# Optimization experiments

Hardware: AMD Instinct MI355X
Metric: run time of the kernel (lower is better)

Reference implementation:

```python
import jax, jax.numpy as jnp
import numpy as np

S, L, D = 128, 512, 256   # MSA rows, residues, msa_dim
H, C = 8, 32              # num_heads, head_dim


def setup_inputs() -> dict:
    key = jax.random.key(0)
    ks = jax.random.split(key, 8)
    inp = {
        "msa_input": jax.random.normal(ks[0], (S, L, D), dtype=jnp.float32),
        "ln_scale": jnp.ones((D,), jnp.float32),
        "ln_bias": jnp.zeros((D,), jnp.float32),
        "wq": jax.random.normal(ks[1], (D, H * C), jnp.float32) / np.sqrt(D),
        "wk": jax.random.normal(ks[2], (D, H * C), jnp.float32) / np.sqrt(D),
        "wv": jax.random.normal(ks[3], (D, H * C), jnp.float32) / np.sqrt(D),
        "wg": jax.random.normal(ks[4], (D, H * C), jnp.float32) / np.sqrt(D),
        "bg": jnp.zeros((H * C,), jnp.float32),
        "wo": jax.random.normal(ks[5], (H * C, D), jnp.float32) / np.sqrt(H * C),
        "bo": jnp.zeros((D,), jnp.float32),
    }
    return inp


def reference(msa_input, ln_scale, ln_bias, wq, wk, wv, wg, bg, wo, bo):
    # LayerNorm over last dim (eps matches torch default 1e-5)
    mu = jnp.mean(msa_input, axis=-1, keepdims=True)
    var = jnp.mean(jnp.square(msa_input - mu), axis=-1, keepdims=True)
    x = (msa_input - mu) * jax.lax.rsqrt(var + 1e-5) * ln_scale + ln_bias

    q = (x @ wq).reshape(S, L, H, C)
    k = (x @ wk).reshape(S, L, H, C)
    v = (x @ wv).reshape(S, L, H, C)
    g = jax.nn.sigmoid(x @ wg + bg).reshape(S, L, H, C)

    scale = 1.0 / np.sqrt(C)
    # attention over MSA-row axis, per residue l and head h
    scores = jnp.einsum("slhc,tlhc->stlh", q, k) * scale   # [S,S,L,H]
    probs = jax.nn.softmax(scores, axis=1)                  # softmax over t
    o = jnp.einsum("stlh,tlhc->slhc", probs, v) * g         # [S,L,H,C]
    return o.reshape(S, L, H * C) @ wo + bo
```

## Files before the change

kernel.cpp:

```cpp
#include <hip/hip_runtime.h>
#include <hip/hip_bf16.h>

typedef __bf16 bf16;
typedef __bf16 bf16x8 __attribute__((ext_vector_type(8)));
typedef float f32x4 __attribute__((ext_vector_type(4)));

#define S_DIM 128
#define L_DIM 512
#define D_DIM 256
#define NQ    1024

__device__ __forceinline__ void gl16(void* lds, const void* g) {
  __builtin_amdgcn_global_load_lds((const __attribute__((address_space(1))) void*)g,
                                   (__attribute__((address_space(3))) void*)lds,
                                   16, 0, 0);
}

__global__ void pack_weights(const float* __restrict__ wq, const float* __restrict__ wk,
                             const float* __restrict__ wv, const float* __restrict__ wg,
                             const float* __restrict__ wo,
                             bf16* __restrict__ wcat_t, bf16* __restrict__ wo_t) {
  int idx = blockIdx.x * 256 + threadIdx.x;
  const int total1 = NQ * D_DIM;
  if (idx < total1) {
    int j = idx >> 8;
    int d = idx & 255;
    const float* w = (j < 256) ? wq : (j < 512) ? wk : (j < 768) ? wv : wg;
    wcat_t[idx] = (bf16)w[d * 256 + (j & 255)];
  } else {
    int i2 = idx - total1;
    if (i2 < D_DIM * D_DIM) {
      int dcol = i2 >> 8, k = i2 & 255;
      wo_t[i2] = (bf16)wo[k * 256 + dcol];
    }
  }
}

__global__ __launch_bounds__(512, 4) void ln_qkvg(const float* __restrict__ msa,
                                                  const float* __restrict__ lns,
                                                  const float* __restrict__ lnb,
                                                  const bf16* __restrict__ wcat,
                                                  const float* __restrict__ bg,
                                                  bf16* __restrict__ pan) {
  __shared__ __align__(16) char smem[65536];
  bf16* Albs = (bf16*)smem;
  char* Bb   = smem;
  const int tid  = threadIdx.x;
  const int wid  = tid >> 6;
  const int lane = tid & 63;
  const int lrow = lane & 15;
  const int lkg  = lane >> 4;
  const int lk   = lkg * 8;
  const int rb   = lkg * 4;
  const int res  = blockIdx.x;

  {
    float4 scv = ((const float4*)lns)[lane];
    float4 bsv = ((const float4*)lnb)[lane];
    const float* mbase = msa + ((size_t)(wid * 16) * 512 + res) * 256 + lane * 4;
    #pragma unroll
    for (int b4 = 0; b4 < 4; ++b4) {
      float4 rv[4];
      #pragma unroll
      for (int i = 0; i < 4; ++i)
        rv[i] = *(const float4*)(mbase + (size_t)(b4 * 4 + i) * 512 * 256);
      #pragma unroll
      for (int i = 0; i < 4; ++i) {
        int s = wid * 16 + b4 * 4 + i;
        float4 v = rv[i];
        float sum = v.x + v.y + v.z + v.w;
        #pragma unroll
        for (int m = 32; m; m >>= 1) sum += __shfl_xor(sum, m);
        float mu = sum * (1.0f / 256.0f);
        float dx = v.x - mu, dy = v.y - mu, dz = v.z - mu, dw = v.w - mu;
        float s2 = dx * dx + dy * dy + dz * dz + dw * dw;
        #pragma unroll
        for (int m = 32; m; m >>= 1) s2 += __shfl_xor(s2, m);
        float rs = rsqrtf(s2 * (1.0f / 256.0f) + 1e-5f);
        union { uint2 u; bf16 b[4]; } o;
        o.b[0] = (bf16)(dx * rs * scv.x + bsv.x);
        o.b[1] = (bf16)(dy * rs * scv.y + bsv.y);
        o.b[2] = (bf16)(dz * rs * scv.z + bsv.z);
        o.b[3] = (bf16)(dw * rs * scv.w + bsv.w);
        *(uint2*)((char*)Albs + (((s * 512) + lane * 8) ^ ((s & 7) << 4))) = o.u;
      }
    }
  }
  __syncthreads();

  const int mq = wid & 3;
  const int nh = wid >> 2;
  bf16x8 afc[2][8];
  #pragma unroll
  for (int mt = 0; mt < 2; ++mt)
    #pragma unroll
    for (int kk = 0; kk < 8; ++kk) {
      int row = mq * 32 + mt * 16 + lrow;
      afc[mt][kk] = *(const bf16x8*)((char*)Albs +
                      (((row * 512) + (kk * 32 + lk) * 2) ^ ((row & 7) << 4)));
    }
  __syncthreads();

  #pragma unroll
  for (int p = 0; p < 4; ++p) {
    int ch = p * 512 + tid;
    int n = ch >> 5;
    int inner = (ch & 31) * 16;
    gl16(Bb + p * 8192 + wid * 1024,
         (const char*)wcat + (size_t)n * 512 + (inner ^ ((n & 7) << 4)));
  }
  __syncthreads();

  const int tb = (mq * 32 + rb) * 64 + nh * 32 + lrow;

  #pragma unroll 1
  for (int cc = 0; cc < 16; ++cc) {
    char* Bcur = Bb + (cc & 1) * 32768;
    if (cc < 15) {
      char* Bnxt = Bb + ((cc + 1) & 1) * 32768;
      const size_t ncol0 = (size_t)(cc + 1) * 64;
      #pragma unroll
      for (int p = 0; p < 4; ++p) {
        int ch = p * 512 + tid;
        int n = ch >> 5;
        int inner = (ch & 31) * 16;
        gl16(Bnxt + p * 8192 + wid * 1024,
             (const char*)wcat + (ncol0 + n) * 512 + (inner ^ ((n & 7) << 4)));
      }
    }
    f32x4 acc[2][2] = {};
    #pragma unroll
    for (int kk = 0; kk < 8; ++kk) {
      bf16x8 bv[2];
      #pragma unroll
      for (int nt = 0; nt < 2; ++nt) {
        int nl = nh * 32 + nt * 16 + lrow;
        bv[nt] = *(const bf16x8*)(Bcur +
                    (((nl * 512) + (kk * 32 + lk) * 2) ^ ((nl & 7) << 4)));
      }
      #pragma unroll
      for (int mt = 0; mt < 2; ++mt)
        #pragma unroll
        for (int nt = 0; nt < 2; ++nt)
          acc[mt][nt] = __builtin_amdgcn_mfma_f32_16x16x32_bf16(afc[mt][kk], bv[nt], acc[mt][nt], 0, 0, 0);
    }
    {
      const bool isg = (cc >= 12);
      const int type = cc >> 2, hp = cc & 3;
      bf16* pstore = pan + ((size_t)((type * 512 + res) * 4) + hp) * 8192 + tb;
      float bgv[2];
      if (isg) {
        bgv[0] = bg[(cc - 12) * 64 + nh * 32 + lrow];
        bgv[1] = bg[(cc - 12) * 64 + nh * 32 + 16 + lrow];
      }
      #pragma unroll
      for (int mt = 0; mt < 2; ++mt)
        #pragma unroll
        for (int nt = 0; nt < 2; ++nt)
          #pragma unroll
          for (int r = 0; r < 4; ++r) {
            float v = acc[mt][nt][r];
            if (isg) { v += bgv[nt]; v = 1.0f / (1.0f + __expf(-v)); }
            pstore[mt * 1024 + r * 64 + nt * 16] = (bf16)v;
          }
    }
    if (cc < 15) {
      asm volatile("s_waitcnt vmcnt(16) lgkmcnt(0)" ::: "memory");
      __builtin_amdgcn_s_barrier();
    }
  }
}

__global__ __launch_bounds__(256, 4) void attn_kernel(const bf16* __restrict__ pan,
                                                      bf16* __restrict__ obuf) {
  __shared__ __align__(16) char smem[40960];
  const int tid  = threadIdx.x;
  const int wid  = tid >> 6;
  const int lane = tid & 63;
  const int lrow = lane & 15;
  const int lkg  = lane >> 4;
  const int lk   = lkg * 8;
  const int rb   = lkg * 4;
  const int bid  = blockIdx.x;
  const int rest = bid >> 3;
  const int hg   = rest & 1;
  const int res  = (bid & 7) | ((rest >> 1) << 3);
  const int h    = hg * 4 + wid;
  const int hp   = h >> 1;
  const int hl   = (h & 1) * 32;

  char* vw  = smem + wid * 8192;
  char* pwb = smem + 32768 + wid * 2048;

  const bf16* Pq = pan + ((size_t)((0 * 512 + res) * 4) + hp) * 8192 + hl;
  const bf16* Pk = pan + ((size_t)((1 * 512 + res) * 4) + hp) * 8192 + hl;
  const bf16* Pv = pan + ((size_t)((2 * 512 + res) * 4) + hp) * 8192 + hl;
  const bf16* Pg = pan + ((size_t)((3 * 512 + res) * 4) + hp) * 8192 + hl;

  {
    int t0 = lane >> 2, cs = (lane & 3) * 8;
    #pragma unroll
    for (int p = 0; p < 8; ++p) {
      int t = p * 16 + t0;
      union { uint4 u; bf16 e[8]; } v;
      v.u = *(const uint4*)(Pv + t * 64 + cs);
      #pragma unroll
      for (int j = 0; j < 8; ++j) {
        int c = cs + j;
        *(bf16*)(vw + ((c * 256 + t * 2) ^ ((c & 7) << 4))) = v.e[j];
      }
    }
  }

  bf16x8 kf[8];
  #pragma unroll
  for (int tt = 0; tt < 8; ++tt)
    kf[tt] = *(const bf16x8*)(Pk + (tt * 16 + lrow) * 64 + lk);

  const float scale = 0.17677669529663687f;
  const f32x4 z = {0.f, 0.f, 0.f, 0.f};

  for (int st = 0; st < 8; ++st) {
    bf16x8 qf = *(const bf16x8*)(Pq + (st * 16 + lrow) * 64 + lk);
    f32x4 sc[8];
    #pragma unroll
    for (int tt = 0; tt < 8; ++tt)
      sc[tt] = __builtin_amdgcn_mfma_f32_16x16x32_bf16(qf, kf[tt], z, 0, 0, 0);

    #pragma unroll
    for (int r = 0; r < 4; ++r) {
      float m = sc[0][r];
      #pragma unroll
      for (int tc = 1; tc < 8; ++tc) m = fmaxf(m, sc[tc][r]);
      #pragma unroll
      for (int msk = 8; msk; msk >>= 1) m = fmaxf(m, __shfl_xor(m, msk));
      float pv[8], ssum = 0.f;
      #pragma unroll
      for (int tc = 0; tc < 8; ++tc) {
        float p = __expf((sc[tc][r] - m) * scale);
        pv[tc] = p; ssum += p;
      }
      #pragma unroll
      for (int msk = 8; msk; msk >>= 1) ssum += __shfl_xor(ssum, msk);
      float inv = 1.0f / ssum;
      #pragma unroll
      for (int tc = 0; tc < 8; ++tc) sc[tc][r] = pv[tc] * inv;
    }

    f32x4 oc[2] = {z, z};
    #pragma unroll
    for (int hf = 0; hf < 2; ++hf) {
      #pragma unroll
      for (int tc = 0; tc < 4; ++tc)
        #pragma unroll
        for (int r = 0; r < 4; ++r) {
          int row = rb + r, col = tc * 16 + lrow;
          *(bf16*)(pwb + ((row * 128 + col * 2) ^ ((row & 7) << 4))) = (bf16)sc[hf * 4 + tc][r];
        }
      #pragma unroll
      for (int kc = 0; kc < 2; ++kc) {
        bf16x8 pa = *(const bf16x8*)(pwb + ((lrow * 128 + (kc * 32 + lk) * 2) ^ ((lrow & 7) << 4)));
        #pragma unroll
        for (int ct = 0; ct < 2; ++ct) {
          int c = ct * 16 + lrow;
          bf16x8 bv = *(const bf16x8*)(vw + ((c * 256 + (hf * 64 + kc * 32 + lk) * 2) ^ ((c & 7) << 4)));
          oc[ct] = __builtin_amdgcn_mfma_f32_16x16x32_bf16(pa, bv, oc[ct], 0, 0, 0);
        }
      }
    }

    #pragma unroll
    for (int ct = 0; ct < 2; ++ct)
      #pragma unroll
      for (int r = 0; r < 4; ++r) {
        int row = rb + r, c = ct * 16 + lrow;
        *(bf16*)(pwb + ((row * 128 + c * 2) ^ ((row & 7) << 4))) = (bf16)oc[ct][r];
      }
    {
      int row = lane >> 2, cb = lane & 3;
      union { uint4 u; bf16 e[8]; } o8, g8, r8;
      o8.u = *(const uint4*)(pwb + ((row * 128 + cb * 16) ^ ((row & 7) << 4)));
      g8.u = *(const uint4*)(Pg + (st * 16 + row) * 64 + cb * 8);
      #pragma unroll
      for (int u = 0; u < 8; ++u) r8.e[u] = (bf16)((float)o8.e[u] * (float)g8.e[u]);
      *(uint4*)(obuf + ((size_t)res * 128 + st * 16 + row) * 256 + h * 32 + cb * 8) = r8.u;
    }
  }
}

__global__ __launch_bounds__(256, 4) void gemm_proj(const bf16* __restrict__ A,
                                                    const bf16* __restrict__ Bt,
                                                    float* __restrict__ Cout,
                                                    const float* __restrict__ bias) {
  __shared__ __align__(16) bf16 smem[16384];
  bf16* As = smem;
  bf16* Bs = smem + 8192;
  const int tid  = threadIdx.x;
  const int wid  = tid >> 6;
  const int lane = tid & 63;
  const int bid   = blockIdx.x;
  const int n_idx = (bid >> 3) & 1;
  const int m_idx = (bid & 7) | ((bid >> 4) << 3);
  const int m0 = m_idx * 128;
  const int n0 = n_idx * 128;
  const int lrow = lane & 15;
  const int lk   = (lane >> 4) * 8;
  const int wr = wid >> 1, wc = wid & 1;

  const int ln8 = lane >> 3;
  const int c8  = ((lane & 7) ^ ln8) * 8;

  const bf16* Arow = A  + (size_t)m0 * 256 + c8;
  const bf16* Brow = Bt + (size_t)n0 * 256 + c8;

  f32x4 acc[4][4] = {};

  #pragma unroll
  for (int ks = 0; ks < 4; ++ks) {
    const int k0 = ks * 64;
    #pragma unroll
    for (int t = 0; t < 4; ++t) {
      int chunk = wid * 4 + t;
      int r = chunk * 8 + ln8;
      gl16(&As[chunk * 512], Arow + (size_t)r * 256 + k0);
      gl16(&Bs[chunk * 512], Brow + (size_t)r * 256 + k0);
    }
    __syncthreads();
    #pragma unroll
    for (int kk = 0; kk < 64; kk += 32) {
      bf16x8 av[4], bv[4];
      #pragma unroll
      for (int i = 0; i < 4; ++i)
        av[i] = *(const bf16x8*)((const char*)As + ((((wr * 64 + i * 16 + lrow) * 128) + (kk + lk) * 2) ^ (((wr * 64 + i * 16 + lrow) & 7) << 4)));
      #pragma unroll
      for (int j = 0; j < 4; ++j)
        bv[j] = *(const bf16x8*)((const char*)Bs + ((((wc * 64 + j * 16 + lrow) * 128) + (kk + lk) * 2) ^ (((wc * 64 + j * 16 + lrow) & 7) << 4)));
      #pragma unroll
      for (int i = 0; i < 4; ++i)
        #pragma unroll
        for (int j = 0; j < 4; ++j)
          acc[i][j] = __builtin_amdgcn_mfma_f32_16x16x32_bf16(av[i], bv[j], acc[i][j], 0, 0, 0);
    }
    __syncthreads();
  }

  const int rb = (lane >> 4) * 4;
  const int xorv = rb << 2;
  float* smf = (float*)smem;
  float bov[4];
  #pragma unroll
  for (int j = 0; j < 4; ++j) bov[j] = bias[n0 + wc * 64 + j * 16 + lrow];
  #pragma unroll
  for (int half = 0; half < 2; ++half) {
    if (half) __syncthreads();
    #pragma unroll
    for (int i2 = 0; i2 < 2; ++i2) {
      int i = half * 2 + i2;
      #pragma unroll
      for (int j = 0; j < 4; ++j) {
        int col = wc * 64 + j * 16 + lrow;
        #pragma unroll
        for (int r = 0; r < 4; ++r) {
          int crow = wr * 32 + i2 * 16 + rb + r;
          smf[crow * 128 + (col ^ xorv)] = acc[i][j][r] + bov[j];
        }
      }
    }
    __syncthreads();
    #pragma unroll
    for (int p = 0; p < 8; ++p) {
      int ch = p * 256 + tid;
      int crow = ch >> 5, slot = (ch & 31) * 4;
      int rx = (crow & 12) << 2;
      int s_loc = (crow >> 5) * 64 + half * 32 + (crow & 31);
      *(uint4*)(Cout + ((size_t)s_loc * 512 + m_idx) * 256 + n0 + slot) =
          *(const uint4*)(smf + crow * 128 + (slot ^ rx));
    }
  }
}

extern "C" void kernel_launch(void* const* d_in, const int* in_sizes, int n_in,
                              void* d_out, int out_size, void* d_ws, size_t ws_size,
                              hipStream_t stream) {
  const float* msa      = (const float*)d_in[0];
  const float* ln_scale = (const float*)d_in[1];
  const float* ln_bias  = (const float*)d_in[2];
  const float* wq       = (const float*)d_in[3];
  const float* wk       = (const float*)d_in[4];
  const float* wv       = (const float*)d_in[5];
  const float* wg       = (const float*)d_in[6];
  const float* bg       = (const float*)d_in[7];
  const float* wo       = (const float*)d_in[8];
  const float* bo       = (const float*)d_in[9];
  float* out = (float*)d_out;

  char* ws = (char*)d_ws;
  bf16* wcat_t = (bf16*)ws;
  bf16* wo_t   = (bf16*)(ws + 524288);
  bf16* pan    = (bf16*)(ws + 655360);
  bf16* obuf   = (bf16*)(ws + 655360 + 134217728ULL);

  pack_weights<<<dim3(1280), dim3(256), 0, stream>>>(wq, wk, wv, wg, wo, wcat_t, wo_t);
  ln_qkvg<<<dim3(512), dim3(512), 0, stream>>>(msa, ln_scale, ln_bias, wcat_t, bg, pan);
  attn_kernel<<<dim3(1024), dim3(256), 0, stream>>>(pan, obuf);
  gemm_proj<<<dim3(1024), dim3(256), 0, stream>>>(obuf, wo_t, out, bo);
}
```

Baseline: 141.1 us.

## Split fused LayerNorm+QKVG kernel into separate LN pass and tiled GEMM

Replaces the fused per-residue LayerNorm+QKVG projection kernel with two kernels. A standalone LN kernel writes bf16 normalized rows, transposed to residue-major, into the output buffer as scratch. A conventional 256x64-tiled GEMM with global-to-LDS loads then computes Q/K/V/G over 4096 blocks. This trades the fused kernel's register-resident A fragments and weight streaming for better parallelism, at the cost of an extra bf16 round trip through global memory and one more kernel launch.

```diff
diff --git a/kernel.cpp b/kernel.cpp
--- a/kernel.cpp
+++ b/kernel.cpp
@@ -36,15 +36,45 @@
   }
 }
 
-__global__ __launch_bounds__(512, 4) void ln_qkvg(const float* __restrict__ msa,
-                                                  const float* __restrict__ lns,
-                                                  const float* __restrict__ lnb,
-                                                  const bf16* __restrict__ wcat,
-                                                  const float* __restrict__ bg,
-                                                  bf16* __restrict__ pan) {
-  __shared__ __align__(16) char smem[65536];
-  bf16* Albs = (bf16*)smem;
-  char* Bb   = smem;
+__global__ __launch_bounds__(256) void ln_kernel(const float* __restrict__ x,
+                                                 const float* __restrict__ sc,
+                                                 const float* __restrict__ bs,
+                                                 bf16* __restrict__ y) {
+  int wid  = threadIdx.x >> 6;
+  int lane = threadIdx.x & 63;
+  int row  = blockIdx.x * 4 + wid;
+  float4 v = ((const float4*)(x + (size_t)row * D_DIM))[lane];
+  float s = v.x + v.y + v.z + v.w;
+  #pragma unroll
+  for (int m = 32; m; m >>= 1) s += __shfl_xor(s, m);
+  float mu = s * (1.0f / 256.0f);
+  float dx = v.x - mu, dy = v.y - mu, dz = v.z - mu, dw = v.w - mu;
+  float s2 = dx * dx + dy * dy + dz * dz + dw * dw;
+  #pragma unroll
+  for (int m = 32; m; m >>= 1) s2 += __shfl_xor(s2, m);
+  float rs = rsqrtf(s2 * (1.0f / 256.0f) + 1e-5f);
+  float4 scv = ((const float4*)sc)[lane];
+  float4 bsv = ((const float4*)bs)[lane];
+  union { uint2 u; bf16 b[4]; } o;
+  o.b[0] = (bf16)(dx * rs * scv.x + bsv.x);
+  o.b[1] = (bf16)(dy * rs * scv.y + bsv.y);
+  o.b[2] = (bf16)(dz * rs * scv.z + bsv.z);
+  o.b[3] = (bf16)(dw * rs * scv.w + bsv.w);
+  int sr = row >> 9, l = row & 511;
+  ((uint2*)y)[(size_t)(l * 128 + sr) * 64 + lane] = o.u;
+}
+
+__device__ __forceinline__ bf16x8 lds_swz(const char* base, int row, int k) {
+  return *(const bf16x8*)(base + (((row << 7) + (k << 1)) ^ ((row & 7) << 4)));
+}
+
+__global__ __launch_bounds__(512, 4) void gemm_qkvg(const bf16* __restrict__ A,
+                                                    const bf16* __restrict__ Bt,
+                                                    bf16* __restrict__ pan,
+                                                    const float* __restrict__ bias) {
+  __shared__ __align__(16) char smem[40960];
+  char* As = smem;
+  char* Bs = smem + 32768;
   const int tid  = threadIdx.x;
   const int wid  = tid >> 6;
   const int lane = tid & 63;
@@ -52,122 +82,71 @@
   const int lkg  = lane >> 4;
   const int lk   = lkg * 8;
   const int rb   = lkg * 4;
-  const int res  = blockIdx.x;
+  const int bid  = blockIdx.x;
+  const int n_idx = (bid >> 3) & 15;
+  const int m_idx = (bid & 7) | ((bid >> 7) << 3);
+  const int m0 = m_idx * 256;
+  const int n0 = n_idx * 64;
+  const int rg = wid >> 1;
+  const int cg = wid & 1;
+
+  const int srow8 = tid >> 3;
+  const int slot  = tid & 7;
+
+  f32x4 acc[4][2] = {};
+
+  #pragma unroll
+  for (int ks = 0; ks < 4; ++ks) {
+    const int k0 = ks * 64;
+    #pragma unroll
+    for (int p = 0; p < 4; ++p) {
+      int r = p * 64 + srow8;
+      gl16(As + p * 8192 + wid * 1024,
+           A + (size_t)(m0 + r) * 256 + k0 + ((slot ^ (r & 7)) * 8));
+    }
+    gl16(Bs + wid * 1024,
+         Bt + (size_t)(n0 + srow8) * 256 + k0 + ((slot ^ (srow8 & 7)) * 8));
+    __syncthreads();
+    #pragma unroll
+    for (int kk = 0; kk < 64; kk += 32) {
+      bf16x8 av[4], bv[2];
+      #pragma unroll
+      for (int i = 0; i < 4; ++i)
+        av[i] = lds_swz(As, rg * 64 + i * 16 + lrow, kk + lk);
+      #pragma unroll
+      for (int nt = 0; nt < 2; ++nt)
+        bv[nt] = lds_swz(Bs, cg * 32 + nt * 16 + lrow, kk + lk);
+      #pragma unroll
+      for (int i = 0; i < 4; ++i)
+        #pragma unroll
+        for (int nt = 0; nt < 2; ++nt)
+          acc[i][nt] = __builtin_amdgcn_mfma_f32_16x16x32_bf16(av[i], bv[nt], acc[i][nt], 0, 0, 0);
+    }
+    if (ks < 3) __syncthreads();
+  }
 
   {
-    float4 scv = ((const float4*)lns)[lane];
-    float4 bsv = ((const float4*)lnb)[lane];
-    const float* mbase = msa + ((size_t)(wid * 16) * 512 + res) * 256 + lane * 4;
-    #pragma unroll
-    for (int b4 = 0; b4 < 4; ++b4) {
-      float4 rv[4];
-      #pragma unroll
-      for (int i = 0; i < 4; ++i)
-        rv[i] = *(const float4*)(mbase + (size_t)(b4 * 4 + i) * 512 * 256);
-      #pragma unroll
-      for (int i = 0; i < 4; ++i) {
-        int s = wid * 16 + b4 * 4 + i;
-        float4 v = rv[i];
-        float sum = v.x + v.y + v.z + v.w;
-        #pragma unroll
-        for (int m = 32; m; m >>= 1) sum += __shfl_xor(sum, m);
-        float mu = sum * (1.0f / 256.0f);
-        float dx = v.x - mu, dy = v.y - mu, dz = v.z - mu, dw = v.w - mu;
-        float s2 = dx * dx + dy * dy + dz * dz + dw * dw;
-        #pragma unroll
-        for (int m = 32; m; m >>= 1) s2 += __shfl_xor(s2, m);
-        float rs = rsqrtf(s2 * (1.0f / 256.0f) + 1e-5f);
-        union { uint2 u; bf16 b[4]; } o;
-        o.b[0] = (bf16)(dx * rs * scv.x + bsv.x);
-        o.b[1] = (bf16)(dy * rs * scv.y + bsv.y);
-        o.b[2] = (bf16)(dz * rs * scv.z + bsv.z);
-        o.b[3] = (bf16)(dw * rs * scv.w + bsv.w);
-        *(uint2*)((char*)Albs + (((s * 512) + lane * 8) ^ ((s & 7) << 4))) = o.u;
-      }
-    }
-  }
-  __syncthreads();
-
-  const int mq = wid & 3;
-  const int nh = wid >> 2;
-  bf16x8 afc[2][8];
-  #pragma unroll
-  for (int mt = 0; mt < 2; ++mt)
-    #pragma unroll
-    for (int kk = 0; kk < 8; ++kk) {
-      int row = mq * 32 + mt * 16 + lrow;
-      afc[mt][kk] = *(const bf16x8*)((char*)Albs +
-                      (((row * 512) + (kk * 32 + lk) * 2) ^ ((row & 7) << 4)));
-    }
-  __syncthreads();
-
-  #pragma unroll
-  for (int p = 0; p < 4; ++p) {
-    int ch = p * 512 + tid;
-    int n = ch >> 5;
-    int inner = (ch & 31) * 16;
-    gl16(Bb + p * 8192 + wid * 1024,
-         (const char*)wcat + (size_t)n * 512 + (inner ^ ((n & 7) << 4)));
-  }
-  __syncthreads();
-
-  const int tb = (mq * 32 + rb) * 64 + nh * 32 + lrow;
-
-  #pragma unroll 1
-  for (int cc = 0; cc < 16; ++cc) {
-    char* Bcur = Bb + (cc & 1) * 32768;
-    if (cc < 15) {
-      char* Bnxt = Bb + ((cc + 1) & 1) * 32768;
-      const size_t ncol0 = (size_t)(cc + 1) * 64;
-      #pragma unroll
-      for (int p = 0; p < 4; ++p) {
-        int ch = p * 512 + tid;
-        int n = ch >> 5;
-        int inner = (ch & 31) * 16;
-        gl16(Bnxt + p * 8192 + wid * 1024,
-             (const char*)wcat + (ncol0 + n) * 512 + (inner ^ ((n & 7) << 4)));
-      }
-    }
-    f32x4 acc[2][2] = {};
-    #pragma unroll
-    for (int kk = 0; kk < 8; ++kk) {
-      bf16x8 bv[2];
-      #pragma unroll
-      for (int nt = 0; nt < 2; ++nt) {
-        int nl = nh * 32 + nt * 16 + lrow;
-        bv[nt] = *(const bf16x8*)(Bcur +
-                    (((nl * 512) + (kk * 32 + lk) * 2) ^ ((nl & 7) << 4)));
-      }
-      #pragma unroll
-      for (int mt = 0; mt < 2; ++mt)
-        #pragma unroll
-        for (int nt = 0; nt < 2; ++nt)
-          acc[mt][nt] = __builtin_amdgcn_mfma_f32_16x16x32_bf16(afc[mt][kk], bv[nt], acc[mt][nt], 0, 0, 0);
-    }
-    {
-      const bool isg = (cc >= 12);
-      const int type = cc >> 2, hp = cc & 3;
-      bf16* pstore = pan + ((size_t)((type * 512 + res) * 4) + hp) * 8192 + tb;
-      float bgv[2];
-      if (isg) {
-        bgv[0] = bg[(cc - 12) * 64 + nh * 32 + lrow];
-        bgv[1] = bg[(cc - 12) * 64 + nh * 32 + 16 + lrow];
-      }
-      #pragma unroll
-      for (int mt = 0; mt < 2; ++mt)
-        #pragma unroll
-        for (int nt = 0; nt < 2; ++nt)
-          #pragma unroll
-          for (int r = 0; r < 4; ++r) {
-            float v = acc[mt][nt][r];
-            if (isg) { v += bgv[nt]; v = 1.0f / (1.0f + __expf(-v)); }
-            pstore[mt * 1024 + r * 64 + nt * 16] = (bf16)v;
-          }
-    }
-    if (cc < 15) {
-      asm volatile("s_waitcnt vmcnt(16) lgkmcnt(0)" ::: "memory");
-      __builtin_amdgcn_s_barrier();
-    }
+    const int type = n_idx >> 2;
+    const int hp   = n_idx & 3;
+    const bool isg = (type == 3);
+    float bgv[2];
+    if (isg) {
+      bgv[0] = bias[(n_idx - 12) * 64 + cg * 32 + lrow];
+      bgv[1] = bias[(n_idx - 12) * 64 + cg * 32 + 16 + lrow];
+    }
+    const int res = m_idx * 2 + (rg >> 1);
+    bf16* pstore = pan + ((size_t)((type * 512 + res) * 4) + hp) * 8192
+                 + ((rg & 1) * 64 + rb) * 64 + cg * 32 + lrow;
+    #pragma unroll
+    for (int i = 0; i < 4; ++i)
+      #pragma unroll
+      for (int nt = 0; nt < 2; ++nt)
+        #pragma unroll
+        for (int r = 0; r < 4; ++r) {
+          float v = acc[i][nt][r];
+          if (isg) { v += bgv[nt]; v = 1.0f / (1.0f + __expf(-v)); }
+          pstore[i * 1024 + r * 64 + nt * 16] = (bf16)v;
+        }
   }
 }
 
@@ -293,8 +272,8 @@
                                                     float* __restrict__ Cout,
                                                     const float* __restrict__ bias) {
   __shared__ __align__(16) bf16 smem[16384];
-  bf16* As = smem;
-  bf16* Bs = smem + 8192;
+  char* As = (char*)smem;
+  char* Bs = (char*)(smem + 8192);
   const int tid  = threadIdx.x;
   const int wid  = tid >> 6;
   const int lane = tid & 63;
@@ -322,8 +301,8 @@
     for (int t = 0; t < 4; ++t) {
       int chunk = wid * 4 + t;
       int r = chunk * 8 + ln8;
-      gl16(&As[chunk * 512], Arow + (size_t)r * 256 + k0);
-      gl16(&Bs[chunk * 512], Brow + (size_t)r * 256 + k0);
+      gl16(As + chunk * 1024, Arow + (size_t)r * 256 + k0);
+      gl16(Bs + chunk * 1024, Brow + (size_t)r * 256 + k0);
     }
     __syncthreads();
     #pragma unroll
@@ -331,10 +310,10 @@
       bf16x8 av[4], bv[4];
       #pragma unroll
       for (int i = 0; i < 4; ++i)
-        av[i] = *(const bf16x8*)((const char*)As + ((((wr * 64 + i * 16 + lrow) * 128) + (kk + lk) * 2) ^ (((wr * 64 + i * 16 + lrow) & 7) << 4)));
+        av[i] = lds_swz(As, wr * 64 + i * 16 + lrow, kk + lk);
       #pragma unroll
       for (int j = 0; j < 4; ++j)
-        bv[j] = *(const bf16x8*)((const char*)Bs + ((((wc * 64 + j * 16 + lrow) * 128) + (kk + lk) * 2) ^ (((wc * 64 + j * 16 + lrow) & 7) << 4)));
+        bv[j] = lds_swz(Bs, wc * 64 + j * 16 + lrow, kk + lk);
       #pragma unroll
       for (int i = 0; i < 4; ++i)
         #pragma unroll
@@ -399,9 +378,11 @@
   bf16* wo_t   = (bf16*)(ws + 524288);
   bf16* pan    = (bf16*)(ws + 655360);
   bf16* obuf   = (bf16*)(ws + 655360 + 134217728ULL);
+  bf16* x_ln2  = (bf16*)d_out;
 
   pack_weights<<<dim3(1280), dim3(256), 0, stream>>>(wq, wk, wv, wg, wo, wcat_t, wo_t);
-  ln_qkvg<<<dim3(512), dim3(512), 0, stream>>>(msa, ln_scale, ln_bias, wcat_t, bg, pan);
+  ln_kernel<<<dim3(65536 / 4), dim3(256), 0, stream>>>(msa, ln_scale, ln_bias, x_ln2);
+  gemm_qkvg<<<dim3(4096), dim3(512), 0, stream>>>(x_ln2, wcat_t, pan, bg);
   attn_kernel<<<dim3(1024), dim3(256), 0, stream>>>(pan, obuf);
   gemm_proj<<<dim3(1024), dim3(256), 0, stream>>>(obuf, wo_t, out, bo);
 }
```

Result: slower. 150.8 us (+6.8%).

## Keep weights in registers and stream LN activations from LDS in QKVG GEMM

Applied to the files above, without the earlier changes.

The fused LayerNorm+QKVG kernel no longer double-buffers weight tiles through LDS with async global->LDS loads and per-chunk barriers. Each wave now owns two 64-column weight panels, loads its 32-column weight slices straight from global memory into registers, and reads the normalized activation rows from LDS for each 16-row sub-tile. This removes the barriers and the LDS weight staging. In exchange, every block issues more direct global weight loads with no prefetch overlap and holds 16 bf16x8 weight fragments in registers per wave. The gemm_proj change only moves the swizzled LDS indexing into a helper.

```diff
diff --git a/kernel.cpp b/kernel.cpp
--- a/kernel.cpp
+++ b/kernel.cpp
@@ -42,9 +42,7 @@
                                                   const bf16* __restrict__ wcat,
                                                   const float* __restrict__ bg,
                                                   bf16* __restrict__ pan) {
-  __shared__ __align__(16) char smem[65536];
-  bf16* Albs = (bf16*)smem;
-  char* Bb   = smem;
+  __shared__ __align__(16) char xlds[65536];
   const int tid  = threadIdx.x;
   const int wid  = tid >> 6;
   const int lane = tid & 63;
@@ -82,93 +80,61 @@
         o.b[1] = (bf16)(dy * rs * scv.y + bsv.y);
         o.b[2] = (bf16)(dz * rs * scv.z + bsv.z);
         o.b[3] = (bf16)(dw * rs * scv.w + bsv.w);
-        *(uint2*)((char*)Albs + (((s * 512) + lane * 8) ^ ((s & 7) << 4))) = o.u;
+        *(uint2*)(xlds + (((s * 512) + lane * 8) ^ ((s & 7) << 4))) = o.u;
       }
     }
   }
   __syncthreads();
 
-  const int mq = wid & 3;
-  const int nh = wid >> 2;
-  bf16x8 afc[2][8];
-  #pragma unroll
-  for (int mt = 0; mt < 2; ++mt)
-    #pragma unroll
-    for (int kk = 0; kk < 8; ++kk) {
-      int row = mq * 32 + mt * 16 + lrow;
-      afc[mt][kk] = *(const bf16x8*)((char*)Albs +
-                      (((row * 512) + (kk * 32 + lk) * 2) ^ ((row & 7) << 4)));
-    }
-  __syncthreads();
-
-  #pragma unroll
-  for (int p = 0; p < 4; ++p) {
-    int ch = p * 512 + tid;
-    int n = ch >> 5;
-    int inner = (ch & 31) * 16;
-    gl16(Bb + p * 8192 + wid * 1024,
-         (const char*)wcat + (size_t)n * 512 + (inner ^ ((n & 7) << 4)));
-  }
-  __syncthreads();
-
-  const int tb = (mq * 32 + rb) * 64 + nh * 32 + lrow;
+  #define LDA(st, kk) (*(const bf16x8*)(xlds + \
+      ((((st) * 16 + lrow) * 512 + ((kk) * 32 + lk) * 2) ^ ((lrow & 7) << 4))))
+
+  const f32x4 z = {0.f, 0.f, 0.f, 0.f};
 
   #pragma unroll 1
-  for (int cc = 0; cc < 16; ++cc) {
-    char* Bcur = Bb + (cc & 1) * 32768;
-    if (cc < 15) {
-      char* Bnxt = Bb + ((cc + 1) & 1) * 32768;
-      const size_t ncol0 = (size_t)(cc + 1) * 64;
-      #pragma unroll
-      for (int p = 0; p < 4; ++p) {
-        int ch = p * 512 + tid;
-        int n = ch >> 5;
-        int inner = (ch & 31) * 16;
-        gl16(Bnxt + p * 8192 + wid * 1024,
-             (const char*)wcat + (ncol0 + n) * 512 + (inner ^ ((n & 7) << 4)));
-      }
-    }
-    f32x4 acc[2][2] = {};
-    #pragma unroll
-    for (int kk = 0; kk < 8; ++kk) {
-      bf16x8 bv[2];
-      #pragma unroll
-      for (int nt = 0; nt < 2; ++nt) {
-        int nl = nh * 32 + nt * 16 + lrow;
-        bv[nt] = *(const bf16x8*)(Bcur +
-                    (((nl * 512) + (kk * 32 + lk) * 2) ^ ((nl & 7) << 4)));
-      }
-      #pragma unroll
-      for (int mt = 0; mt < 2; ++mt)
-        #pragma unroll
-        for (int nt = 0; nt < 2; ++nt)
-          acc[mt][nt] = __builtin_amdgcn_mfma_f32_16x16x32_bf16(afc[mt][kk], bv[nt], acc[mt][nt], 0, 0, 0);
-    }
-    {
-      const bool isg = (cc >= 12);
-      const int type = cc >> 2, hp = cc & 3;
-      bf16* pstore = pan + ((size_t)((type * 512 + res) * 4) + hp) * 8192 + tb;
+  for (int np = 0; np < 2; ++np) {
+    const int n_idx = np * 8 + wid;
+    const int type  = n_idx >> 2;
+    const int hp    = n_idx & 3;
+    const bool isg  = (n_idx >= 12);
+    #pragma unroll 1
+    for (int nc = 0; nc < 2; ++nc) {
+      bf16x8 bw[2][8];
+      #pragma unroll
+      for (int cg = 0; cg < 2; ++cg)
+        #pragma unroll
+        for (int kk = 0; kk < 8; ++kk)
+          bw[cg][kk] = *(const bf16x8*)(wcat +
+              (size_t)(n_idx * 64 + nc * 32 + cg * 16 + lrow) * 256 + kk * 32 + lk);
       float bgv[2];
       if (isg) {
-        bgv[0] = bg[(cc - 12) * 64 + nh * 32 + lrow];
-        bgv[1] = bg[(cc - 12) * 64 + nh * 32 + 16 + lrow];
-      }
-      #pragma unroll
-      for (int mt = 0; mt < 2; ++mt)
-        #pragma unroll
-        for (int nt = 0; nt < 2; ++nt)
-          #pragma unroll
-          for (int r = 0; r < 4; ++r) {
-            float v = acc[mt][nt][r];
-            if (isg) { v += bgv[nt]; v = 1.0f / (1.0f + __expf(-v)); }
-            pstore[mt * 1024 + r * 64 + nt * 16] = (bf16)v;
+        bgv[0] = bg[(n_idx - 12) * 64 + nc * 32 + lrow];
+        bgv[1] = bg[(n_idx - 12) * 64 + nc * 32 + 16 + lrow];
+      }
+      bf16* pst = pan + ((size_t)((type * 512 + res) * 4) + hp) * 8192 + nc * 32 + lrow;
+      #pragma unroll
+      for (int st = 0; st < 8; ++st) {
+        f32x4 c0 = z, c1 = z;
+        #pragma unroll
+        for (int kk = 0; kk < 8; ++kk) {
+          bf16x8 a = LDA(st, kk);
+          c0 = __builtin_amdgcn_mfma_f32_16x16x32_bf16(a, bw[0][kk], c0, 0, 0, 0);
+          c1 = __builtin_amdgcn_mfma_f32_16x16x32_bf16(a, bw[1][kk], c1, 0, 0, 0);
+        }
+        #pragma unroll
+        for (int r = 0; r < 4; ++r) {
+          float v0 = c0[r], v1 = c1[r];
+          if (isg) {
+            v0 = 1.0f / (1.0f + __expf(-(v0 + bgv[0])));
+            v1 = 1.0f / (1.0f + __expf(-(v1 + bgv[1])));
           }
-    }
-    if (cc < 15) {
-      asm volatile("s_waitcnt vmcnt(16) lgkmcnt(0)" ::: "memory");
-      __builtin_amdgcn_s_barrier();
-    }
-  }
+          pst[(st * 16 + rb + r) * 64]      = (bf16)v0;
+          pst[(st * 16 + rb + r) * 64 + 16] = (bf16)v1;
+        }
+      }
+    }
+  }
+  #undef LDA
 }
 
 __global__ __launch_bounds__(256, 4) void attn_kernel(const bf16* __restrict__ pan,
@@ -288,13 +254,17 @@
   }
 }
 
+__device__ __forceinline__ bf16x8 lds_swz(const char* base, int row, int k) {
+  return *(const bf16x8*)(base + (((row << 7) + (k << 1)) ^ ((row & 7) << 4)));
+}
+
 __global__ __launch_bounds__(256, 4) void gemm_proj(const bf16* __restrict__ A,
                                                     const bf16* __restrict__ Bt,
                                                     float* __restrict__ Cout,
                                                     const float* __restrict__ bias) {
   __shared__ __align__(16) bf16 smem[16384];
-  bf16* As = smem;
-  bf16* Bs = smem + 8192;
+  char* As = (char*)smem;
+  char* Bs = (char*)(smem + 8192);
   const int tid  = threadIdx.x;
   const int wid  = tid >> 6;
   const int lane = tid & 63;
@@ -322,8 +292,8 @@
     for (int t = 0; t < 4; ++t) {
       int chunk = wid * 4 + t;
       int r = chunk * 8 + ln8;
-      gl16(&As[chunk * 512], Arow + (size_t)r * 256 + k0);
-      gl16(&Bs[chunk * 512], Brow + (size_t)r * 256 + k0);
+      gl16(As + chunk * 1024, Arow + (size_t)r * 256 + k0);
+      gl16(Bs + chunk * 1024, Brow + (size_t)r * 256 + k0);
     }
     __syncthreads();
     #pragma unroll
@@ -331,10 +301,10 @@
       bf16x8 av[4], bv[4];
       #pragma unroll
       for (int i = 0; i < 4; ++i)
-        av[i] = *(const bf16x8*)((const char*)As + ((((wr * 64 + i * 16 + lrow) * 128) + (kk + lk) * 2) ^ (((wr * 64 + i * 16 + lrow) & 7) << 4)));
+        av[i] = lds_swz(As, wr * 64 + i * 16 + lrow, kk + lk);
       #pragma unroll
       for (int j = 0; j < 4; ++j)
-        bv[j] = *(const bf16x8*)((const char*)Bs + ((((wc * 64 + j * 16 + lrow) * 128) + (kk + lk) * 2) ^ (((wc * 64 + j * 16 + lrow) & 7) << 4)));
+        bv[j] = lds_swz(Bs, wc * 64 + j * 16 + lrow, kk + lk);
       #pragma unroll
       for (int i = 0; i < 4; ++i)
         #pragma unroll
```

New measurement: 303.5 us. 115% more time.
